# Optimization experiments

Hardware: AMD Instinct MI355X
Metric: run time of the kernel (lower is better)

## Reference

```python
import jax, jax.numpy as jnp
import numpy as np

NUM_LAYERS = 4   # i: conv layers in Unary
K_DISP = 128     # k: disparity labels
FEAT_C = 64      # unary feature channels


def _conv3x3(x, w, b):
    # x: [B,C,H,W], w: [O,I,3,3] (OIHW), padding SAME, stride 1
    y = jax.lax.conv_general_dilated(
        x, w, window_strides=(1, 1), padding='SAME',
        dimension_numbers=('NCHW', 'OIHW', 'NCHW'))
    return y + b[None, :, None, None]


def _unary(x, Ws, bs):
    # i conv layers, tanh between layers, linear output (siamese unary net)
    n = len(Ws)
    for i in range(n):
        x = _conv3x3(x, Ws[i], bs[i])
        if i < n - 1:
            x = jnp.tanh(x)
    return x


def _correlation(phiL, phiR, k):
    # corr[b,d,y,x] = sum_c phiL[b,c,y,x] * phiR[b,c,y,x-d], zero out-of-range
    B, C, H, W = phiL.shape
    Rpad = jnp.pad(phiR, ((0, 0), (0, 0), (0, 0), (k - 1, 0)))  # zero-pad left

    def step(_, d):
        # shifted right feature map: Rpad[..., k-1-d : k-1-d+W] == phiR shifted right by d
        Rs = jax.lax.dynamic_slice_in_dim(Rpad, k - 1 - d, W, axis=3)
        return None, jnp.einsum('bchw,bchw->bhw', phiL, Rs)

    _, ys = jax.lax.scan(step, None, jnp.arange(k))  # [k,B,H,W]
    return jnp.moveaxis(ys, 0, 1)                    # [B,k,H,W]


def setup_inputs() -> dict:
    key = jax.random.key(0)
    ks = jax.random.split(key, 2 + NUM_LAYERS)
    B, H, W = 2, 384, 1280
    d = {
        'l': jax.random.normal(ks[0], (B, 3, H, W), jnp.float32),
        'r': jax.random.normal(ks[1], (B, 3, H, W), jnp.float32),
    }
    chans = [3] + [FEAT_C] * NUM_LAYERS

    def xavier(k_, shape):
        fan_in = shape[1] * shape[2] * shape[3]
        fan_out = shape[0] * shape[2] * shape[3]
        std = float(np.sqrt(2.0 / (fan_in + fan_out)))
        return jax.random.normal(k_, shape, jnp.float32) * std

    for i in range(NUM_LAYERS):
        d[f'W{i}'] = xavier(ks[2 + i], (chans[i + 1], chans[i], 3, 3))
        d[f'b{i}'] = jnp.zeros((chans[i + 1],), jnp.float32)
    return d


def reference(l, r, W0, b0, W1, b1, W2, b2, W3, b3):
    Ws = [W0, W1, W2, W3]
    bs = [b0, b1, b2, b3]
    phi_left = _unary(l, Ws, bs)
    phi_right = _unary(r, Ws, bs)
    return _correlation(phi_left, phi_right, K_DISP)  # [B, k, H, W]
```

## Files before the change

kernel.cpp:

```cpp
#include <hip/hip_runtime.h>

#define HH 384
#define WW 1280

typedef unsigned short u16;
typedef unsigned int u32;
typedef __attribute__((ext_vector_type(8))) short short8;
typedef __attribute__((ext_vector_type(8))) unsigned short u16x8;
typedef __attribute__((ext_vector_type(4))) float f32x4;

__device__ __forceinline__ float bf2f(u16 u){ union{u32 i;float f;}v; v.i=((u32)u)<<16; return v.f; }
__device__ __forceinline__ u16 f2bf(float f){ union{float f;u32 i;}v; v.f=f; u32 r=v.i+0x7fffu+((v.i>>16)&1u); return (u16)(r>>16); }
__device__ __forceinline__ float ftanh(float x){
  float e = __expf(2.0f*x);
  return 1.0f - 2.0f/(e+1.0f);
}
__device__ __forceinline__ void gload_lds16(const void* g, void* l){
  __builtin_amdgcn_global_load_lds((const __attribute__((address_space(1))) void*)g,
                                   (__attribute__((address_space(3))) void*)l, 16, 0, 0);
}

__global__ __launch_bounds__(256) void prep_weights(const float* __restrict__ W1,
    const float* __restrict__ W2, const float* __restrict__ W3, u16* __restrict__ wf){
  int idx = blockIdx.x*256 + threadIdx.x;
  if (idx >= 110592) return;
  int m    = idx & 63;
  int oc   = (idx>>6) & 63;
  int tap  = (idx>>12) % 9;
  int layer= idx / 36864;
  int ic   = m ^ ((oc&7)<<3);
  const float* Ws = layer==0 ? W1 : (layer==1 ? W2 : W3);
  wf[idx] = f2bf(Ws[(oc*64+ic)*9 + tap]);
}

__global__ __launch_bounds__(256) void conv0_kernel(const float* __restrict__ img,
    const float* __restrict__ W0, const float* __restrict__ b0, u16* __restrict__ out){
  int x = blockIdx.x*256 + threadIdx.x;
  int y = blockIdx.y;
  int n = blockIdx.z;
  const float* in = img + (size_t)n*3*HH*WW;
  float acc[64];
  #pragma unroll
  for (int o=0;o<64;++o) acc[o] = b0[o];
  #pragma unroll
  for (int ic=0; ic<3; ++ic)
  #pragma unroll
  for (int dy=0; dy<3; ++dy){
    int gy = y + dy - 1;
    #pragma unroll
    for (int dx=0; dx<3; ++dx){
      int gx = x + dx - 1;
      float v = 0.f;
      if (gy>=0 && gy<HH && (unsigned)gx < (unsigned)WW)
        v = in[((size_t)ic*HH + gy)*WW + gx];
      #pragma unroll
      for (int o=0;o<64;++o)
        acc[o] = fmaf(v, W0[(o*3+ic)*9 + dy*3 + dx], acc[o]);
    }
  }
  u16* op = out + ((size_t)((n*HH + y)*WW) + x)*64;
  #pragma unroll
  for (int cc=0; cc<8; ++cc){
    u16x8 v;
    #pragma unroll
    for (int k=0;k<8;++k) v[k] = f2bf(ftanh(acc[cc*8+k]));
    *(u16x8*)(op + cc*8) = v;
  }
}

template<bool TANH>
__global__ __launch_bounds__(256) void conv64_kernel(const u16* __restrict__ in,
    const u16* __restrict__ wfL, const float* __restrict__ bias,
    const u16* __restrict__ zpad, u16* __restrict__ out){
  __shared__ u16 tile[6*66*64];
  __shared__ u16 wbuf[3][4096];
  const int tid = threadIdx.x;
  const int x0 = blockIdx.x*64;
  const int y0 = blockIdx.y*4;
  const int n  = blockIdx.z;
  const u16* inN = in + (size_t)n*HH*WW*64;

  for (int q0 = 0; q0 < 3168; q0 += 256){
    int q = q0 + tid;
    if (q < 3168){
      int row = q / 528;
      int rem = q - row*528;
      int col = rem >> 3;
      int j   = rem & 7;
      int gy = y0 - 1 + row;
      int gx = x0 - 1 + col;
      const u16* g;
      if ((unsigned)gy < (unsigned)HH && (unsigned)gx < (unsigned)WW)
        g = inN + (((size_t)(gy*WW + gx))<<6) + ((j ^ (col&7))<<3);
      else
        g = zpad + (j<<3);
      gload_lds16(g, &tile[(size_t)(q & ~63)*8]);
    }
  }
  #pragma unroll
  for (int t=0; t<2; ++t)
    #pragma unroll
    for (int c=0; c<2; ++c){
      int q = c*256 + tid;
      gload_lds16(wfL + (size_t)t*4096 + (size_t)q*8, &wbuf[t][(q & ~63)*8]);
    }
  asm volatile("s_waitcnt vmcnt(2)" ::: "memory");
  __builtin_amdgcn_s_barrier();
  __builtin_amdgcn_sched_barrier(0);

  const int lane = tid & 63;
  const int wv = tid >> 6;
  const int l15 = lane & 15;
  const int lh  = lane >> 4;

  f32x4 acc[4][4];
  #pragma unroll
  for (int mt=0;mt<4;++mt)
    #pragma unroll
    for (int nt=0;nt<4;++nt) acc[mt][nt] = (f32x4){0.f,0.f,0.f,0.f};

  #pragma unroll
  for (int tap = 0; tap < 9; ++tap){
    const int dy = tap/3, dx = tap%3;
    if (tap <= 6){
      const u16* wsrc = wfL + (size_t)(tap+2)*4096;
      u16* wdst = wbuf[(tap+2)%3];
      #pragma unroll
      for (int c=0;c<2;++c){
        int q = c*256 + tid;
        gload_lds16(wsrc + (size_t)q*8, &wdst[(q & ~63)*8]);
      }
    }
    const char* wb = (const char*)wbuf[tap%3];
    const char* tb = (const char*)tile;
    const int xorA = ((l15 + dx)&7)<<4;
    const int xorB = (l15&7)<<4;
    #pragma unroll
    for (int kh=0; kh<2; ++kh){
      const int kbyte = kh*64 + lh*16;
      short8 a[4], b[4];
      #pragma unroll
      for (int mt=0; mt<4; ++mt){
        int col = mt*16 + l15 + dx;
        a[mt] = *(const short8*)(tb + ((wv+dy)*66 + col)*128 + (kbyte ^ xorA));
      }
      #pragma unroll
      for (int nt=0; nt<4; ++nt){
        int oc = nt*16 + l15;
        b[nt] = *(const short8*)(wb + oc*128 + (kbyte ^ xorB));
      }
      #pragma unroll
      for (int mt=0; mt<4; ++mt)
        #pragma unroll
        for (int nt=0; nt<4; ++nt)
          acc[mt][nt] = __builtin_amdgcn_mfma_f32_16x16x32_bf16(a[mt], b[nt], acc[mt][nt], 0,0,0);
    }
    if (tap < 8){
      if (tap <= 6) asm volatile("s_waitcnt vmcnt(2)" ::: "memory");
      else          asm volatile("s_waitcnt vmcnt(0)" ::: "memory");
      __builtin_amdgcn_s_barrier();
      __builtin_amdgcn_sched_barrier(0);
    }
  }

  float bv[4];
  #pragma unroll
  for (int nt=0;nt<4;++nt) bv[nt] = bias[nt*16 + l15];
  const int gy = y0 + wv;
  u16* outR = out + (size_t)n*HH*WW*64 + (size_t)gy*WW*64;
  #pragma unroll
  for (int mt=0; mt<4; ++mt){
    #pragma unroll
    for (int r=0; r<4; ++r){
      int x = x0 + mt*16 + lh*4 + r;
      u16* op = outR + (size_t)x*64 + l15;
      #pragma unroll
      for (int nt=0; nt<4; ++nt){
        float v = acc[mt][nt][r] + bv[nt];
        if (TANH) v = ftanh(v);
        op[nt*16] = f2bf(v);
      }
    }
  }
}

__global__ __launch_bounds__(256) void corr_kernel(const u16* __restrict__ phiL,
    const u16* __restrict__ phiR, const u16* __restrict__ zpad, float* __restrict__ out){
  __shared__ char lds[33280];
  u16* Lt = (u16*)lds;
  u16* Rt = (u16*)(lds + 8192);
  float* band = (float*)lds;
  const int tid = threadIdx.x;
  const int x0 = blockIdx.x*64;
  const int y  = blockIdx.y;
  const int b  = blockIdx.z;
  const u16* Lrow = phiL + ((size_t)(b*HH + y)*WW)*64;
  const u16* Rrow = phiR + ((size_t)(b*HH + y)*WW)*64;

  #pragma unroll
  for (int c0=0; c0<2; ++c0){
    int q = c0*256 + tid;
    int x = q>>3, j = q&7;
    const u16* g = Lrow + (((size_t)(x0 + x))<<6) + ((j ^ (x&7))<<3);
    gload_lds16(g, &Lt[(q & ~63)*8]);
  }
  #pragma unroll
  for (int c0=0; c0<6; ++c0){
    int q = c0*256 + tid;
    int jr = q>>3, j = q&7;
    int gx = x0 - 128 + jr;
    const u16* g = (gx >= 0) ? (Rrow + (((size_t)gx)<<6) + ((j ^ (jr&7))<<3))
                             : (zpad + (j<<3));
    gload_lds16(g, &Rt[(q & ~63)*8]);
  }
  __syncthreads();

  const int lane = tid & 63;
  const int wv   = tid >> 6;
  const int l15  = lane & 15;
  const int lh   = lane >> 4;
  const int xorS = (l15&7)<<4;

  f32x4 acc[4][3];
  #pragma unroll
  for (int mt=0;mt<4;++mt)
    #pragma unroll
    for (int nt=0;nt<3;++nt) acc[mt][nt] = (f32x4){0.f,0.f,0.f,0.f};

  const char* tbL = (const char*)Lt;
  const char* tbR = (const char*)Rt;
  #pragma unroll
  for (int kh=0; kh<2; ++kh){
    const int kbyte = kh*64 + lh*16;
    short8 a[4], bb[3];
    #pragma unroll
    for (int mt=0; mt<4; ++mt)
      a[mt] = *(const short8*)(tbL + (mt*16 + l15)*128 + (kbyte ^ xorS));
    #pragma unroll
    for (int nt=0; nt<3; ++nt)
      bb[nt] = *(const short8*)(tbR + (wv*48 + nt*16 + l15)*128 + (kbyte ^ xorS));
    #pragma unroll
    for (int mt=0; mt<4; ++mt)
      #pragma unroll
      for (int nt=0; nt<3; ++nt)
        acc[mt][nt] = __builtin_amdgcn_mfma_f32_16x16x32_bf16(a[mt], bb[nt], acc[mt][nt], 0,0,0);
  }
  __syncthreads();

  #pragma unroll
  for (int mt=0; mt<4; ++mt){
    #pragma unroll
    for (int nt=0; nt<3; ++nt){
      int jr = wv*48 + nt*16 + l15;
      #pragma unroll
      for (int r=0; r<4; ++r){
        int x = mt*16 + lh*4 + r;
        int d = x - jr + 128;
        if ((unsigned)d < 128u) band[d*65 + x] = acc[mt][nt][r];
      }
    }
  }
  __syncthreads();

  float* ob = out + ((size_t)(b*128)*HH + (size_t)y)*WW + x0;
  #pragma unroll
  for (int it=0; it<8; ++it){
    int c = it*256 + tid;
    int d = c>>4, xq = c&15;
    const float* bp = &band[d*65 + xq*4];
    float4 v = make_float4(bp[0], bp[1], bp[2], bp[3]);
    *(float4*)&ob[(size_t)d*HH*WW + xq*4] = v;
  }
}

extern "C" void kernel_launch(void* const* d_in, const int* in_sizes, int n_in,
                              void* d_out, int out_size, void* d_ws, size_t ws_size,
                              hipStream_t stream){
  const float* l  = (const float*)d_in[0];
  const float* r  = (const float*)d_in[1];
  const float* W0 = (const float*)d_in[2];
  const float* b0 = (const float*)d_in[3];
  const float* W1 = (const float*)d_in[4];
  const float* b1 = (const float*)d_in[5];
  const float* W2 = (const float*)d_in[6];
  const float* b2 = (const float*)d_in[7];
  const float* W3 = (const float*)d_in[8];
  const float* b3 = (const float*)d_in[9];
  float* out = (float*)d_out;

  const size_t SIDE = (size_t)2*HH*WW*64;
  u16* wf   = (u16*)d_ws;
  u16* zpad = (u16*)((char*)d_ws + (1u<<20));
  u16* BL   = (u16*)((char*)d_ws + (2u<<20));
  u16* BR   = BL + SIDE;
  u16* A    = (u16*)d_out;

  hipMemsetAsync(zpad, 0, 256, stream);
  prep_weights<<<dim3(432), dim3(256), 0, stream>>>(W1, W2, W3, wf);

  for (int s = 0; s < 2; ++s){
    const float* img = s ? r : l;
    u16* B = s ? BR : BL;
    conv0_kernel<<<dim3(WW/256, HH, 2), dim3(256), 0, stream>>>(img, W0, b0, A);
    conv64_kernel<true ><<<dim3(WW/64, HH/4, 2), dim3(256), 0, stream>>>(A, wf + 0*36864, b1, zpad, B);
    conv64_kernel<true ><<<dim3(WW/64, HH/4, 2), dim3(256), 0, stream>>>(B, wf + 1*36864, b2, zpad, A);
    conv64_kernel<false><<<dim3(WW/64, HH/4, 2), dim3(256), 0, stream>>>(A, wf + 2*36864, b3, zpad, B);
  }

  corr_kernel<<<dim3(WW/64, HH, 2), dim3(256), 0, stream>>>(BL, BR, zpad, out);
}
```

Measured before the change: 1.046 ms.

## Split conv64 K dimension across waves with LDS reduction, halve rows per block

The conv64 kernel now covers 2 output rows per block instead of 4. The four waves are split as 2 rows × 2 K-halves, and the partial accumulators are reduced through LDS before the bias, tanh and store step. The weight buffer goes from triple to double buffering, each tap waits on vmcnt(0), and launch bounds ask for 3 blocks per CU. This aims at higher occupancy and more blocks in flight. In exchange it re-reads more halo rows per output row, adds an LDS reduction with extra barriers, and has less prefetch depth for the weights.

Measured after the change: 1.190 ms. 13.7% more time.

```diff
diff --git a/kernel.cpp b/kernel.cpp
--- a/kernel.cpp
+++ b/kernel.cpp
@@ -69,20 +69,21 @@
 }
 
 template<bool TANH>
-__global__ __launch_bounds__(256) void conv64_kernel(const u16* __restrict__ in,
+__global__ __launch_bounds__(256, 3) void conv64_kernel(const u16* __restrict__ in,
     const u16* __restrict__ wfL, const float* __restrict__ bias,
     const u16* __restrict__ zpad, u16* __restrict__ out){
-  __shared__ u16 tile[6*66*64];
-  __shared__ u16 wbuf[3][4096];
+  __shared__ __align__(16) char tilebuf[34816];
+  __shared__ __align__(16) u16 wbuf[2][4096];
+  u16* tile = (u16*)tilebuf;
   const int tid = threadIdx.x;
   const int x0 = blockIdx.x*64;
-  const int y0 = blockIdx.y*4;
+  const int y0 = blockIdx.y*2;
   const int n  = blockIdx.z;
   const u16* inN = in + (size_t)n*HH*WW*64;
 
-  for (int q0 = 0; q0 < 3168; q0 += 256){
+  for (int q0 = 0; q0 < 2112; q0 += 256){
     int q = q0 + tid;
-    if (q < 3168){
+    if (q < 2112){
       int row = q / 528;
       int rem = q - row*528;
       int col = rem >> 3;
@@ -109,9 +110,13 @@
   __builtin_amdgcn_sched_barrier(0);
 
   const int lane = tid & 63;
-  const int wv = tid >> 6;
+  const int wv  = tid >> 6;
+  const int yr  = wv & 1;
+  const int kh  = wv >> 1;
   const int l15 = lane & 15;
   const int lh  = lane >> 4;
+  const int kbyte = kh*64 + lh*16;
+  const int xorB  = (l15&7)<<4;
 
   f32x4 acc[4][4];
   #pragma unroll
@@ -122,63 +127,70 @@
   #pragma unroll
   for (int tap = 0; tap < 9; ++tap){
     const int dy = tap/3, dx = tap%3;
-    if (tap <= 6){
-      const u16* wsrc = wfL + (size_t)(tap+2)*4096;
-      u16* wdst = wbuf[(tap+2)%3];
+    if (tap >= 1 && tap < 8){
+      const u16* wsrc = wfL + (size_t)(tap+1)*4096;
+      u16* wdst = wbuf[(tap+1)&1];
       #pragma unroll
       for (int c=0;c<2;++c){
         int q = c*256 + tid;
         gload_lds16(wsrc + (size_t)q*8, &wdst[(q & ~63)*8]);
       }
     }
-    const char* wb = (const char*)wbuf[tap%3];
+    const char* wb = (const char*)wbuf[tap&1];
     const char* tb = (const char*)tile;
     const int xorA = ((l15 + dx)&7)<<4;
-    const int xorB = (l15&7)<<4;
-    #pragma unroll
-    for (int kh=0; kh<2; ++kh){
-      const int kbyte = kh*64 + lh*16;
-      short8 a[4], b[4];
-      #pragma unroll
-      for (int mt=0; mt<4; ++mt){
-        int col = mt*16 + l15 + dx;
-        a[mt] = *(const short8*)(tb + ((wv+dy)*66 + col)*128 + (kbyte ^ xorA));
-      }
-      #pragma unroll
-      for (int nt=0; nt<4; ++nt){
-        int oc = nt*16 + l15;
-        b[nt] = *(const short8*)(wb + oc*128 + (kbyte ^ xorB));
-      }
-      #pragma unroll
-      for (int mt=0; mt<4; ++mt)
-        #pragma unroll
-        for (int nt=0; nt<4; ++nt)
-          acc[mt][nt] = __builtin_amdgcn_mfma_f32_16x16x32_bf16(a[mt], b[nt], acc[mt][nt], 0,0,0);
-    }
+    short8 a[4], w[4];
+    #pragma unroll
+    for (int mt=0; mt<4; ++mt){
+      int col = mt*16 + l15 + dx;
+      a[mt] = *(const short8*)(tb + ((yr+dy)*66 + col)*128 + (kbyte ^ xorA));
+    }
+    #pragma unroll
+    for (int nt=0; nt<4; ++nt)
+      w[nt] = *(const short8*)(wb + (nt*16+l15)*128 + (kbyte ^ xorB));
+    #pragma unroll
+    for (int mt=0; mt<4; ++mt)
+      #pragma unroll
+      for (int nt=0; nt<4; ++nt)
+        acc[mt][nt] = __builtin_amdgcn_mfma_f32_16x16x32_bf16(a[mt], w[nt], acc[mt][nt], 0,0,0);
     if (tap < 8){
-      if (tap <= 6) asm volatile("s_waitcnt vmcnt(2)" ::: "memory");
-      else          asm volatile("s_waitcnt vmcnt(0)" ::: "memory");
+      asm volatile("s_waitcnt vmcnt(0)" ::: "memory");
       __builtin_amdgcn_s_barrier();
       __builtin_amdgcn_sched_barrier(0);
     }
   }
 
-  float bv[4];
-  #pragma unroll
-  for (int nt=0;nt<4;++nt) bv[nt] = bias[nt*16 + l15];
-  const int gy = y0 + wv;
-  u16* outR = out + (size_t)n*HH*WW*64 + (size_t)gy*WW*64;
-  #pragma unroll
-  for (int mt=0; mt<4; ++mt){
-    #pragma unroll
-    for (int r=0; r<4; ++r){
-      int x = x0 + mt*16 + lh*4 + r;
-      u16* op = outR + (size_t)x*64 + l15;
+  __syncthreads();
+  float* red = (float*)tilebuf;
+  if (kh == 1){
+    #pragma unroll
+    for (int mt=0; mt<4; ++mt)
       #pragma unroll
       for (int nt=0; nt<4; ++nt){
-        float v = acc[mt][nt][r] + bv[nt];
-        if (TANH) v = ftanh(v);
-        op[nt*16] = f2bf(v);
+        int off = (yr*64 + nt*16 + l15)*68 + mt*16 + lh*4;
+        *(f32x4*)&red[off] = acc[mt][nt];
+      }
+  }
+  __syncthreads();
+  if (kh == 0){
+    float bv[4];
+    #pragma unroll
+    for (int nt=0;nt<4;++nt) bv[nt] = bias[nt*16 + l15];
+    const int gy = y0 + yr;
+    u16* outR = out + (size_t)n*HH*WW*64 + (size_t)gy*WW*64;
+    #pragma unroll
+    for (int mt=0; mt<4; ++mt){
+      #pragma unroll
+      for (int nt=0; nt<4; ++nt){
+        int off = (yr*64 + nt*16 + l15)*68 + mt*16 + lh*4;
+        f32x4 p = *(const f32x4*)&red[off];
+        #pragma unroll
+        for (int r=0; r<4; ++r){
+          int x = x0 + mt*16 + lh*4 + r;
+          float v = acc[mt][nt][r] + p[r] + bv[nt];
+          if (TANH) v = ftanh(v);
+          outR[(size_t)x*64 + nt*16 + l15] = f2bf(v);
+        }
       }
     }
   }
@@ -186,7 +198,7 @@
 
 __global__ __launch_bounds__(256) void corr_kernel(const u16* __restrict__ phiL,
     const u16* __restrict__ phiR, const u16* __restrict__ zpad, float* __restrict__ out){
-  __shared__ char lds[33280];
+  __shared__ __align__(16) char lds[33280];
   u16* Lt = (u16*)lds;
   u16* Rt = (u16*)(lds + 8192);
   float* band = (float*)lds;
@@ -302,9 +314,9 @@
     const float* img = s ? r : l;
     u16* B = s ? BR : BL;
     conv0_kernel<<<dim3(WW/256, HH, 2), dim3(256), 0, stream>>>(img, W0, b0, A);
-    conv64_kernel<true ><<<dim3(WW/64, HH/4, 2), dim3(256), 0, stream>>>(A, wf + 0*36864, b1, zpad, B);
-    conv64_kernel<true ><<<dim3(WW/64, HH/4, 2), dim3(256), 0, stream>>>(B, wf + 1*36864, b2, zpad, A);
-    conv64_kernel<false><<<dim3(WW/64, HH/4, 2), dim3(256), 0, stream>>>(A, wf + 2*36864, b3, zpad, B);
+    conv64_kernel<true ><<<dim3(WW/64, HH/2, 2), dim3(256), 0, stream>>>(A, wf + 0*36864, b1, zpad, B);
+    conv64_kernel<true ><<<dim3(WW/64, HH/2, 2), dim3(256), 0, stream>>>(B, wf + 1*36864, b2, zpad, A);
+    conv64_kernel<false><<<dim3(WW/64, HH/2, 2), dim3(256), 0, stream>>>(A, wf + 2*36864, b3, zpad, B);
   }
 
   corr_kernel<<<dim3(WW/64, HH, 2), dim3(256), 0, stream>>>(BL, BR, zpad, out);
```

## Remap block IDs for XCD locality and load corr operands directly from global

Applied to the files above, without the earlier changes.

Both conv64 and corr kernels now use a 1D grid with an XCD-aware block index swizzle, so consecutive blocks on the same XCD handle neighbouring tiles and share L2. The correlation kernel drops the LDS staging of the L and R features. Each wave now reads its MFMA operands straight from global memory (relying on cache), with zero fill for out-of-range columns. This removes a barrier and cuts LDS use, but it adds redundant, uncoalesced global reads across waves.

After: 1.044 ms. Within noise of the previous version (-0.2%).

```diff
diff --git a/kernel.cpp b/kernel.cpp
--- a/kernel.cpp
+++ b/kernel.cpp
@@ -72,12 +72,14 @@
 __global__ __launch_bounds__(256) void conv64_kernel(const u16* __restrict__ in,
     const u16* __restrict__ wfL, const float* __restrict__ bias,
     const u16* __restrict__ zpad, u16* __restrict__ out){
-  __shared__ u16 tile[6*66*64];
-  __shared__ u16 wbuf[3][4096];
+  __shared__ __align__(16) u16 tile[6*66*64];
+  __shared__ __align__(16) u16 wbuf[3][4096];
   const int tid = threadIdx.x;
-  const int x0 = blockIdx.x*64;
-  const int y0 = blockIdx.y*4;
-  const int n  = blockIdx.z;
+  int id = blockIdx.x;
+  id = (id & 7)*480 + (id >> 3);
+  const int x0 = (id % 20)*64;
+  const int y0 = ((id / 20) % 96)*4;
+  const int n  = id / 1920;
   const u16* inN = in + (size_t)n*HH*WW*64;
 
   for (int q0 = 0; q0 < 3168; q0 += 256){
@@ -185,41 +187,21 @@
 }
 
 __global__ __launch_bounds__(256) void corr_kernel(const u16* __restrict__ phiL,
-    const u16* __restrict__ phiR, const u16* __restrict__ zpad, float* __restrict__ out){
-  __shared__ char lds[33280];
-  u16* Lt = (u16*)lds;
-  u16* Rt = (u16*)(lds + 8192);
-  float* band = (float*)lds;
+    const u16* __restrict__ phiR, float* __restrict__ out){
+  __shared__ __align__(16) float band[128*65];
   const int tid = threadIdx.x;
-  const int x0 = blockIdx.x*64;
-  const int y  = blockIdx.y;
-  const int b  = blockIdx.z;
+  int id = blockIdx.x;
+  id = (id & 7)*1920 + (id >> 3);
+  const int x0 = (id % 20)*64;
+  const int y  = (id / 20) % 384;
+  const int b  = id / 7680;
   const u16* Lrow = phiL + ((size_t)(b*HH + y)*WW)*64;
   const u16* Rrow = phiR + ((size_t)(b*HH + y)*WW)*64;
-
-  #pragma unroll
-  for (int c0=0; c0<2; ++c0){
-    int q = c0*256 + tid;
-    int x = q>>3, j = q&7;
-    const u16* g = Lrow + (((size_t)(x0 + x))<<6) + ((j ^ (x&7))<<3);
-    gload_lds16(g, &Lt[(q & ~63)*8]);
-  }
-  #pragma unroll
-  for (int c0=0; c0<6; ++c0){
-    int q = c0*256 + tid;
-    int jr = q>>3, j = q&7;
-    int gx = x0 - 128 + jr;
-    const u16* g = (gx >= 0) ? (Rrow + (((size_t)gx)<<6) + ((j ^ (jr&7))<<3))
-                             : (zpad + (j<<3));
-    gload_lds16(g, &Rt[(q & ~63)*8]);
-  }
-  __syncthreads();
 
   const int lane = tid & 63;
   const int wv   = tid >> 6;
   const int l15  = lane & 15;
   const int lh   = lane >> 4;
-  const int xorS = (l15&7)<<4;
 
   f32x4 acc[4][3];
   #pragma unroll
@@ -227,25 +209,25 @@
     #pragma unroll
     for (int nt=0;nt<3;++nt) acc[mt][nt] = (f32x4){0.f,0.f,0.f,0.f};
 
-  const char* tbL = (const char*)Lt;
-  const char* tbR = (const char*)Rt;
   #pragma unroll
   for (int kh=0; kh<2; ++kh){
-    const int kbyte = kh*64 + lh*16;
+    const int koff = kh*32 + lh*8;
     short8 a[4], bb[3];
     #pragma unroll
     for (int mt=0; mt<4; ++mt)
-      a[mt] = *(const short8*)(tbL + (mt*16 + l15)*128 + (kbyte ^ xorS));
-    #pragma unroll
-    for (int nt=0; nt<3; ++nt)
-      bb[nt] = *(const short8*)(tbR + (wv*48 + nt*16 + l15)*128 + (kbyte ^ xorS));
+      a[mt] = *(const short8*)(Lrow + (size_t)(x0 + mt*16 + l15)*64 + koff);
+    #pragma unroll
+    for (int nt=0; nt<3; ++nt){
+      int gx = x0 - 128 + wv*48 + nt*16 + l15;
+      short8 z = (short8){0,0,0,0,0,0,0,0};
+      bb[nt] = (gx >= 0) ? *(const short8*)(Rrow + (size_t)gx*64 + koff) : z;
+    }
     #pragma unroll
     for (int mt=0; mt<4; ++mt)
       #pragma unroll
       for (int nt=0; nt<3; ++nt)
         acc[mt][nt] = __builtin_amdgcn_mfma_f32_16x16x32_bf16(a[mt], bb[nt], acc[mt][nt], 0,0,0);
   }
-  __syncthreads();
 
   #pragma unroll
   for (int mt=0; mt<4; ++mt){
@@ -302,10 +284,10 @@
     const float* img = s ? r : l;
     u16* B = s ? BR : BL;
     conv0_kernel<<<dim3(WW/256, HH, 2), dim3(256), 0, stream>>>(img, W0, b0, A);
-    conv64_kernel<true ><<<dim3(WW/64, HH/4, 2), dim3(256), 0, stream>>>(A, wf + 0*36864, b1, zpad, B);
-    conv64_kernel<true ><<<dim3(WW/64, HH/4, 2), dim3(256), 0, stream>>>(B, wf + 1*36864, b2, zpad, A);
-    conv64_kernel<false><<<dim3(WW/64, HH/4, 2), dim3(256), 0, stream>>>(A, wf + 2*36864, b3, zpad, B);
-  }
-
-  corr_kernel<<<dim3(WW/64, HH, 2), dim3(256), 0, stream>>>(BL, BR, zpad, out);
-}
+    conv64_kernel<true ><<<dim3(3840), dim3(256), 0, stream>>>(A, wf + 0*36864, b1, zpad, B);
+    conv64_kernel<true ><<<dim3(3840), dim3(256), 0, stream>>>(B, wf + 1*36864, b2, zpad, A);
+    conv64_kernel<false><<<dim3(3840), dim3(256), 0, stream>>>(A, wf + 2*36864, b3, zpad, B);
+  }
+
+  corr_kernel<<<dim3(15360), dim3(256), 0, stream>>>(BL, BR, out);
+}
```
